# Optimization experiments

Hardware: AMD Instinct MI355X
Metric: run time of the kernel (lower is better)

## Reference

```python
import jax, jax.numpy as jnp
import numpy as np

HIDDEN = 1024
HEADS = 16
HEAD_DIM = HIDDEN // HEADS  # 64
BLOCK = 1024  # block_size; seq_len > BLOCK triggers ring path
B, S = 1, 4096


def setup_inputs() -> dict:
    key = jax.random.key(0)
    k0, k1, k2, k3, k4 = jax.random.split(key, 5)
    w_scale = 0.02
    return {
        "hidden_states": jax.random.normal(k0, (B, S, HIDDEN), dtype=jnp.float32),
        # weights stored [in, out]; applied as x @ W (equivalent to nn.Linear with W.T)
        "w_q": jax.random.normal(k1, (HIDDEN, HIDDEN), dtype=jnp.float32) * w_scale,
        "w_k": jax.random.normal(k2, (HIDDEN, HIDDEN), dtype=jnp.float32) * w_scale,
        "w_v": jax.random.normal(k3, (HIDDEN, HIDDEN), dtype=jnp.float32) * w_scale,
        "w_o": jax.random.normal(k4, (HIDDEN, HIDDEN), dtype=jnp.float32) * w_scale,
    }


def _ring_attention(q, k, v, block, scale):
    # q,k,v: [B, H, S, D]. Faithful to the torch module: each KV block subtracts
    # its OWN local max (no running-max rescale); exp-sums and weighted-V are
    # accumulated additively across KV blocks, then normalized once at the end.
    b, h, s, d = q.shape
    nb = s // block
    kb = jnp.moveaxis(k.reshape(b, h, nb, block, d), 2, 0)  # [nb, B, H, block, D]
    vb = jnp.moveaxis(v.reshape(b, h, nb, block, d), 2, 0)

    def step(carry, kv):
        num, den = carry
        k_blk, v_blk = kv
        s_blk = jnp.einsum("bhqd,bhkd->bhqk", q, k_blk) * scale  # [B,H,S,block]
        m = jnp.max(s_blk, axis=-1, keepdims=True)               # local max only
        e = jnp.exp(s_blk - m)
        num = num + jnp.einsum("bhqk,bhkd->bhqd", e, v_blk)
        den = den + jnp.sum(e, axis=-1, keepdims=True)
        return (num, den), None

    init = (jnp.zeros_like(q), jnp.zeros((b, h, s, 1), dtype=q.dtype))
    (num, den), _ = jax.lax.scan(step, init, (kb, vb))
    return num / den


def reference(hidden_states, w_q, w_k, w_v, w_o):
    b, s, _ = hidden_states.shape
    q = (hidden_states @ w_q).reshape(b, s, HEADS, HEAD_DIM).transpose(0, 2, 1, 3)
    k = (hidden_states @ w_k).reshape(b, s, HEADS, HEAD_DIM).transpose(0, 2, 1, 3)
    v = (hidden_states @ w_v).reshape(b, s, HEADS, HEAD_DIM).transpose(0, 2, 1, 3)
    scale = HEAD_DIM ** -0.5
    out = _ring_attention(q, k, v, BLOCK, scale)          # [B,H,S,D]
    out = out.transpose(0, 2, 1, 3).reshape(b, s, HIDDEN)  # [B,S,hidden]
    return out @ w_o
```

## Files before the change

### kernel.cpp

```cpp
#include <hip/hip_runtime.h>
#include <hip/hip_bf16.h>

typedef __bf16 bf16;
typedef bf16 bf16x2 __attribute__((ext_vector_type(2)));
typedef bf16 bf16x4 __attribute__((ext_vector_type(4)));
typedef bf16 bf16x8 __attribute__((ext_vector_type(8)));
typedef float f32x4 __attribute__((ext_vector_type(4)));

#define HID 1024
#define NHEADS 16
#define HD 64
#define SEQ 4096

__device__ __forceinline__ void gll16(const void* g, void* l) {
  __builtin_amdgcn_global_load_lds(
      (const __attribute__((address_space(1))) void*)g,
      (__attribute__((address_space(3))) void*)l, 16, 0, 0);
}

__device__ __forceinline__ float fast_exp2(float x) {
#if __has_builtin(__builtin_amdgcn_exp2f)
  return __builtin_amdgcn_exp2f(x);
#else
  return __expf(x * 0.6931471805599453f);
#endif
}

__global__ __launch_bounds__(256)
void prep_kernel(const float* __restrict__ X,
                 const float* __restrict__ Wq, const float* __restrict__ Wk,
                 const float* __restrict__ Wv, const float* __restrict__ Wo,
                 bf16* __restrict__ Xb, bf16* __restrict__ Wt)
{
  const int z = blockIdx.z, t = threadIdx.x, bx = blockIdx.x;
  if (z == 0) {
    const float4* src = (const float4*)X;
    const int gid = bx * 256 + t;
    #pragma unroll
    for (int i = 0; i < 16; ++i) {
      float4 v = src[gid + i * 65536];
      bf16x4 o = {(bf16)v.x, (bf16)v.y, (bf16)v.z, (bf16)v.w};
      *(bf16x4*)&Xb[(size_t)(gid + i * 65536) * 4] = o;
    }
  } else {
    const float* W = (z == 1) ? Wq : (z == 2) ? Wk : (z == 3) ? Wv : Wo;
    bf16* dst = Wt + (size_t)(z - 1) * HID * HID;
    const float scale = (z == 1) ? 0.18033688011112042f : 1.0f;
    __shared__ bf16 T[64][68];
    const int tr = (bx >> 4) * 64, tc = (bx & 15) * 64;
    #pragma unroll
    for (int p = 0; p < 4; ++p) {
      int row = (t >> 4) + p * 16;
      float4 v = *(const float4*)&W[(size_t)(tr + row) * HID + tc + (t & 15) * 4];
      T[row][(t & 15) * 4 + 0] = (bf16)(v.x * scale);
      T[row][(t & 15) * 4 + 1] = (bf16)(v.y * scale);
      T[row][(t & 15) * 4 + 2] = (bf16)(v.z * scale);
      T[row][(t & 15) * 4 + 3] = (bf16)(v.w * scale);
    }
    __syncthreads();
    #pragma unroll
    for (int p = 0; p < 4; ++p) {
      int rp = (t >> 4) + p * 16;
      int cb = (t & 15) * 4;
      bf16x4 o = {T[cb + 0][rp], T[cb + 1][rp], T[cb + 2][rp], T[cb + 3][rp]};
      *(bf16x4*)&dst[(size_t)(tc + rp) * HID + tr + cb] = o;
    }
  }
}

__global__ __launch_bounds__(256)
void qkv_gemm(const bf16* __restrict__ A, const bf16* __restrict__ Wt,
              bf16* __restrict__ Qg, bf16* __restrict__ Kg,
              bf16* __restrict__ Vt)
{
  __shared__ bf16 sbuf[16384];
  bf16* As = sbuf;
  bf16* Bs = sbuf + 8192;

  const int t = threadIdx.x, lane = t & 63, w = t >> 6;
  const int z = blockIdx.z;
  const int n0 = blockIdx.x * 128, m0 = blockIdx.y * 128;
  const bf16* Bt = Wt + (size_t)z * HID * HID;
  const int wm = (w & 1) * 64, wn = (w >> 1) * 64;
  const int fr = lane & 15, quad = lane >> 4;

  f32x4 acc[4][4] = {};

  const int sr = lane >> 3;
  const int sc = ((lane & 7) - sr) & 7;
  const bf16* ga = A  + (size_t)(m0 + w * 32 + sr) * HID + sc * 8;
  const bf16* gb = Bt + (size_t)(n0 + w * 32 + sr) * HID + sc * 8;

  for (int k0 = 0; k0 < HID; k0 += 64) {
    __syncthreads();
    #pragma unroll
    for (int c = 0; c < 4; ++c) {
      gll16(ga + (size_t)(c * 8) * HID + k0, As + (w * 32 + c * 8) * 64);
      gll16(gb + (size_t)(c * 8) * HID + k0, Bs + (w * 32 + c * 8) * 64);
    }
    __syncthreads();
    #pragma unroll
    for (int ks = 0; ks < 2; ++ks) {
      bf16x8 af[4], bg[4];
      #pragma unroll
      for (int i = 0; i < 4; ++i)
        af[i] = *(const bf16x8*)&As[(wm + i * 16 + fr) * 64 +
                                    ((ks * 4 + quad + fr) & 7) * 8];
      #pragma unroll
      for (int i = 0; i < 4; ++i)
        bg[i] = *(const bf16x8*)&Bs[(wn + i * 16 + fr) * 64 +
                                    ((ks * 4 + quad + fr) & 7) * 8];
      #pragma unroll
      for (int mi = 0; mi < 4; ++mi)
        #pragma unroll
        for (int ni = 0; ni < 4; ++ni)
          acc[mi][ni] = __builtin_amdgcn_mfma_f32_16x16x32_bf16(
              af[mi], bg[ni], acc[mi][ni], 0, 0, 0);
    }
  }

  if (z < 2) {
    bf16* C = z ? Kg : Qg;
    #pragma unroll
    for (int mi = 0; mi < 4; ++mi)
      #pragma unroll
      for (int ni = 0; ni < 4; ++ni)
        #pragma unroll
        for (int r = 0; r < 4; ++r)
          C[(size_t)(m0 + wm + mi * 16 + quad * 4 + r) * HID +
            n0 + wn + ni * 16 + fr] = (bf16)acc[mi][ni][r];
  } else {
    __syncthreads();
    #pragma unroll
    for (int mi = 0; mi < 4; ++mi)
      #pragma unroll
      for (int ni = 0; ni < 4; ++ni)
        #pragma unroll
        for (int r = 0; r < 4; ++r) {
          int row = wn + ni * 16 + fr;
          int col = wm + mi * 16 + quad * 4 + r;
          int colS = (col + 8 * (row & 15)) & 127;
          sbuf[row * 128 + colS] = (bf16)acc[mi][ni][r];
        }
    __syncthreads();
    const int row = t >> 1, cb = (t & 1) * 64;
    #pragma unroll
    for (int j = 0; j < 8; ++j) {
      int c0 = (cb + j * 8 + 8 * (row & 15)) & 127;
      *(bf16x8*)&Vt[(size_t)(n0 + row) * SEQ + m0 + cb + j * 8] =
          *(const bf16x8*)&sbuf[row * 128 + c0];
    }
  }
}

__global__ __launch_bounds__(256)
void oproj_gemm(const bf16* __restrict__ A, const bf16* __restrict__ Bt,
                float* __restrict__ C)
{
  __shared__ bf16 sbuf[16384];
  bf16* As = sbuf;
  bf16* Bs = sbuf + 8192;

  const int t = threadIdx.x, lane = t & 63, w = t >> 6;
  const int n0 = blockIdx.x * 128, m0 = blockIdx.y * 128;
  const int wm = (w & 1) * 64, wn = (w >> 1) * 64;
  const int fr = lane & 15, quad = lane >> 4;

  f32x4 acc[4][4] = {};

  const int sr = lane >> 3;
  const int sc = ((lane & 7) - sr) & 7;
  const bf16* ga = A  + (size_t)(m0 + w * 32 + sr) * HID + sc * 8;
  const bf16* gb = Bt + (size_t)(n0 + w * 32 + sr) * HID + sc * 8;

  for (int k0 = 0; k0 < HID; k0 += 64) {
    __syncthreads();
    #pragma unroll
    for (int c = 0; c < 4; ++c) {
      gll16(ga + (size_t)(c * 8) * HID + k0, As + (w * 32 + c * 8) * 64);
      gll16(gb + (size_t)(c * 8) * HID + k0, Bs + (w * 32 + c * 8) * 64);
    }
    __syncthreads();
    #pragma unroll
    for (int ks = 0; ks < 2; ++ks) {
      bf16x8 af[4], bg[4];
      #pragma unroll
      for (int i = 0; i < 4; ++i)
        af[i] = *(const bf16x8*)&As[(wm + i * 16 + fr) * 64 +
                                    ((ks * 4 + quad + fr) & 7) * 8];
      #pragma unroll
      for (int i = 0; i < 4; ++i)
        bg[i] = *(const bf16x8*)&Bs[(wn + i * 16 + fr) * 64 +
                                    ((ks * 4 + quad + fr) & 7) * 8];
      #pragma unroll
      for (int mi = 0; mi < 4; ++mi)
        #pragma unroll
        for (int ni = 0; ni < 4; ++ni)
          acc[mi][ni] = __builtin_amdgcn_mfma_f32_16x16x32_bf16(
              af[mi], bg[ni], acc[mi][ni], 0, 0, 0);
    }
  }

  #pragma unroll
  for (int mi = 0; mi < 4; ++mi)
    #pragma unroll
    for (int ni = 0; ni < 4; ++ni)
      #pragma unroll
      for (int r = 0; r < 4; ++r)
        C[(size_t)(m0 + wm + mi * 16 + quad * 4 + r) * HID +
          n0 + wn + ni * 16 + fr] = acc[mi][ni][r];
}

#define THR_L2 12.0f

__global__ __launch_bounds__(256, 4)
void attn6(const bf16* __restrict__ Q, const bf16* __restrict__ K,
           const bf16* __restrict__ Vt, float* __restrict__ Num,
           float* __restrict__ Den)
{
  __shared__ bf16 Ks[2][4096];
  __shared__ bf16 Vs[2][4096];
  __shared__ bf16 Ps[4][1024];

  const int t = threadIdx.x, lane = t & 63, w = t >> 6;
  const int h = blockIdx.y, q0 = blockIdx.x * 128, half = blockIdx.z;
  const int fr = lane & 15, quad = lane >> 4;

  bf16x8 bq[2][2];
  #pragma unroll
  for (int qf = 0; qf < 2; ++qf)
    #pragma unroll
    for (int ks = 0; ks < 2; ++ks)
      bq[qf][ks] = *(const bf16x8*)&Q[(size_t)(q0 + w * 32 + qf * 16 + fr) * HID
                                      + h * 64 + ks * 32 + quad * 8];

  const int sr = lane >> 3;
  const int sc = ((lane & 7) - sr) & 7;
  const bf16* gk = K  + (size_t)(half * 2048 + w * 16 + sr) * HID + h * 64 + sc * 8;
  const bf16* gv = Vt + (size_t)(h * 64 + w * 16 + sr) * SEQ + half * 2048 + sc * 8;

  #pragma unroll
  for (int j = 0; j < 2; ++j) {
    gll16(gk + (size_t)(j * 8) * HID, &Ks[0][(w * 16 + j * 8) * 64]);
    gll16(gv + (size_t)(j * 8) * SEQ, &Vs[0][(w * 16 + j * 8) * 64]);
  }

  f32x4 accN[2][4] = {};
  f32x4 accO[2][4] = {};
  float m_used[2] = {-3e38f, -3e38f}, m_true[2] = {-3e38f, -3e38f};
  float l_i[2] = {0.f, 0.f}, den[2] = {0.f, 0.f};

  __syncthreads();

  for (int kk = 0; kk < 32; ++kk) {
    const int buf = kk & 1;
    if (kk < 31) {
      const size_t key0n = (size_t)(kk + 1) * 64;
      #pragma unroll
      for (int j = 0; j < 2; ++j) {
        gll16(gk + (key0n + j * 8) * HID, &Ks[buf ^ 1][(w * 16 + j * 8) * 64]);
        gll16(gv + key0n + (size_t)(j * 8) * SEQ,
              &Vs[buf ^ 1][(w * 16 + j * 8) * 64]);
      }
    }

    bf16x8 ak[4][2];
    #pragma unroll
    for (int mt = 0; mt < 4; ++mt)
      #pragma unroll
      for (int ks = 0; ks < 2; ++ks)
        ak[mt][ks] = *(const bf16x8*)&Ks[buf][(mt * 16 + fr) * 64 +
                                             ((ks * 4 + quad + fr) & 7) * 8];

    f32x4 s[2][4];
    #pragma unroll
    for (int qf = 0; qf < 2; ++qf)
      #pragma unroll
      for (int mt = 0; mt < 4; ++mt) {
        f32x4 z = {};
        z = __builtin_amdgcn_mfma_f32_16x16x32_bf16(ak[mt][0], bq[qf][0], z, 0, 0, 0);
        z = __builtin_amdgcn_mfma_f32_16x16x32_bf16(ak[mt][1], bq[qf][1], z, 0, 0, 0);
        s[qf][mt] = z;
      }

    bf16x8 bp[2][2];
    #pragma unroll
    for (int qf = 0; qf < 2; ++qf) {
      float mx0 = fmaxf(fmaxf(s[qf][0][0], s[qf][0][1]), fmaxf(s[qf][0][2], s[qf][0][3]));
      float mx1 = fmaxf(fmaxf(s[qf][1][0], s[qf][1][1]), fmaxf(s[qf][1][2], s[qf][1][3]));
      float mx2 = fmaxf(fmaxf(s[qf][2][0], s[qf][2][1]), fmaxf(s[qf][2][2], s[qf][2][3]));
      float mx3 = fmaxf(fmaxf(s[qf][3][0], s[qf][3][1]), fmaxf(s[qf][3][2], s[qf][3][3]));
      float mx = fmaxf(fmaxf(mx0, mx1), fmaxf(mx2, mx3));
      mx = fmaxf(mx, __shfl_xor(mx, 16));
      mx = fmaxf(mx, __shfl_xor(mx, 32));
      m_true[qf] = fmaxf(m_true[qf], mx);

      if (__any(mx > m_used[qf] + THR_L2)) {
        const float mn = fmaxf(m_used[qf], mx);
        const float a = fast_exp2(m_used[qf] - mn);
        m_used[qf] = mn;
        l_i[qf] *= a;
        #pragma unroll
        for (int dt = 0; dt < 4; ++dt) accO[qf][dt] *= a;
      }

      float sum = 0.f;
      const int prow = fr * 64;
      #pragma unroll
      for (int mt = 0; mt < 4; ++mt) {
        float p0 = fast_exp2(s[qf][mt][0] - m_used[qf]);
        float p1 = fast_exp2(s[qf][mt][1] - m_used[qf]);
        float p2 = fast_exp2(s[qf][mt][2] - m_used[qf]);
        float p3 = fast_exp2(s[qf][mt][3] - m_used[qf]);
        sum += (p0 + p1) + (p2 + p3);
        bf16x4 pv = {(bf16)p0, (bf16)p1, (bf16)p2, (bf16)p3};
        *(bf16x4*)&Ps[w][prow + ((mt * 2 + (quad >> 1) + fr) & 7) * 8 +
                         (quad & 1) * 4] = pv;
      }
      sum += __shfl_xor(sum, 16);
      sum += __shfl_xor(sum, 32);
      l_i[qf] += sum;

      #pragma unroll
      for (int ks = 0; ks < 2; ++ks)
        bp[qf][ks] = *(const bf16x8*)&Ps[w][fr * 64 +
                                            ((ks * 4 + quad + fr) & 7) * 8];
    }

    #pragma unroll
    for (int ks = 0; ks < 2; ++ks)
      #pragma unroll
      for (int dt = 0; dt < 4; ++dt) {
        bf16x8 av = *(const bf16x8*)&Vs[buf][(dt * 16 + fr) * 64 +
                                            ((ks * 4 + quad + fr) & 7) * 8];
        accO[0][dt] = __builtin_amdgcn_mfma_f32_16x16x32_bf16(av, bp[0][ks], accO[0][dt], 0, 0, 0);
        accO[1][dt] = __builtin_amdgcn_mfma_f32_16x16x32_bf16(av, bp[1][ks], accO[1][dt], 0, 0, 0);
      }

    if ((kk & 15) == 15) {
      #pragma unroll
      for (int qf = 0; qf < 2; ++qf) {
        const float c = fast_exp2(m_used[qf] - m_true[qf]);
        den[qf] += l_i[qf] * c;
        #pragma unroll
        for (int dt = 0; dt < 4; ++dt)
          #pragma unroll
          for (int r = 0; r < 4; ++r) accN[qf][dt][r] += accO[qf][dt][r] * c;
        #pragma unroll
        for (int dt = 0; dt < 4; ++dt) accO[qf][dt] = (f32x4){0.f, 0.f, 0.f, 0.f};
        l_i[qf] = 0.f; m_used[qf] = -3e38f; m_true[qf] = -3e38f;
      }
    }
    __syncthreads();
  }

  float* numH = Num + (size_t)half * SEQ * HID;
  #pragma unroll
  for (int qf = 0; qf < 2; ++qf) {
    const int qrow = q0 + w * 32 + qf * 16 + fr;
    const size_t orow = (size_t)qrow * HID + h * 64;
    #pragma unroll
    for (int dt = 0; dt < 4; ++dt)
      *(f32x4*)&numH[orow + dt * 16 + quad * 4] = accN[qf][dt];
    if (quad == 0)
      Den[((size_t)half * 16 + h) * SEQ + qrow] = den[qf];
  }
}

__global__ __launch_bounds__(256)
void combine_kernel(const float* __restrict__ Num, const float* __restrict__ Den,
                    bf16* __restrict__ Og)
{
  const int gid = blockIdx.x * 256 + threadIdx.x;
  const int idx = gid * 4;
  const int row = idx >> 10, col = idx & 1023, h = col >> 6;
  const float d0 = Den[(size_t)h * SEQ + row];
  const float d1 = Den[((size_t)16 + h) * SEQ + row];
  const float inv = 1.0f / (d0 + d1);
  f32x4 a = *(const f32x4*)&Num[idx];
  f32x4 b = *(const f32x4*)&Num[(size_t)SEQ * HID + idx];
  bf16x4 o = {(bf16)((a[0] + b[0]) * inv), (bf16)((a[1] + b[1]) * inv),
              (bf16)((a[2] + b[2]) * inv), (bf16)((a[3] + b[3]) * inv)};
  *(bf16x4*)&Og[idx] = o;
}

__global__ __launch_bounds__(256, 2)
void attn5(const bf16* __restrict__ Q, const bf16* __restrict__ K,
           const bf16* __restrict__ Vt, bf16* __restrict__ O)
{
  __shared__ bf16 Ks[2][4096];
  __shared__ bf16 Vs[2][4096];
  __shared__ bf16 Ps[4][1024];

  const int t = threadIdx.x, lane = t & 63, w = t >> 6;
  const int h = blockIdx.y, q0 = blockIdx.x * 128;
  const int fr = lane & 15, quad = lane >> 4;

  bf16x8 bq[2][2];
  #pragma unroll
  for (int qf = 0; qf < 2; ++qf)
    #pragma unroll
    for (int ks = 0; ks < 2; ++ks)
      bq[qf][ks] = *(const bf16x8*)&Q[(size_t)(q0 + w * 32 + qf * 16 + fr) * HID
                                      + h * 64 + ks * 32 + quad * 8];

  const int sr = lane >> 3;
  const int sc = ((lane & 7) - sr) & 7;
  const bf16* gk = K  + (size_t)(w * 16 + sr) * HID + h * 64 + sc * 8;
  const bf16* gv = Vt + (size_t)(h * 64 + w * 16 + sr) * SEQ + sc * 8;

  #pragma unroll
  for (int j = 0; j < 2; ++j) {
    gll16(gk + (size_t)(j * 8) * HID, &Ks[0][(w * 16 + j * 8) * 64]);
    gll16(gv + (size_t)(j * 8) * SEQ, &Vs[0][(w * 16 + j * 8) * 64]);
  }

  f32x4 accN[2][4] = {};
  f32x4 accO[2][4] = {};
  float m_used[2] = {-3e38f, -3e38f}, m_true[2] = {-3e38f, -3e38f};
  float l_i[2] = {0.f, 0.f}, den[2] = {0.f, 0.f};

  __syncthreads();

  for (int kk = 0; kk < 64; ++kk) {
    const int buf = kk & 1;
    if (kk < 63) {
      const size_t key0n = (size_t)(kk + 1) * 64;
      #pragma unroll
      for (int j = 0; j < 2; ++j) {
        gll16(gk + (key0n + j * 8) * HID, &Ks[buf ^ 1][(w * 16 + j * 8) * 64]);
        gll16(gv + key0n + (size_t)(j * 8) * SEQ,
              &Vs[buf ^ 1][(w * 16 + j * 8) * 64]);
      }
    }

    bf16x8 ak[4][2];
    #pragma unroll
    for (int mt = 0; mt < 4; ++mt)
      #pragma unroll
      for (int ks = 0; ks < 2; ++ks)
        ak[mt][ks] = *(const bf16x8*)&Ks[buf][(mt * 16 + fr) * 64 +
                                             ((ks * 4 + quad + fr) & 7) * 8];

    f32x4 s[2][4];
    #pragma unroll
    for (int qf = 0; qf < 2; ++qf)
      #pragma unroll
      for (int mt = 0; mt < 4; ++mt) {
        f32x4 z = {};
        z = __builtin_amdgcn_mfma_f32_16x16x32_bf16(ak[mt][0], bq[qf][0], z, 0, 0, 0);
        z = __builtin_amdgcn_mfma_f32_16x16x32_bf16(ak[mt][1], bq[qf][1], z, 0, 0, 0);
        s[qf][mt] = z;
      }

    bf16x8 bp[2][2];
    #pragma unroll
    for (int qf = 0; qf < 2; ++qf) {
      float mx0 = fmaxf(fmaxf(s[qf][0][0], s[qf][0][1]), fmaxf(s[qf][0][2], s[qf][0][3]));
      float mx1 = fmaxf(fmaxf(s[qf][1][0], s[qf][1][1]), fmaxf(s[qf][1][2], s[qf][1][3]));
      float mx2 = fmaxf(fmaxf(s[qf][2][0], s[qf][2][1]), fmaxf(s[qf][2][2], s[qf][2][3]));
      float mx3 = fmaxf(fmaxf(s[qf][3][0], s[qf][3][1]), fmaxf(s[qf][3][2], s[qf][3][3]));
      float mx = fmaxf(fmaxf(mx0, mx1), fmaxf(mx2, mx3));
      mx = fmaxf(mx, __shfl_xor(mx, 16));
      mx = fmaxf(mx, __shfl_xor(mx, 32));
      m_true[qf] = fmaxf(m_true[qf], mx);

      if (__any(mx > m_used[qf] + THR_L2)) {
        const float mn = fmaxf(m_used[qf], mx);
        const float a = fast_exp2(m_used[qf] - mn);
        m_used[qf] = mn;
        l_i[qf] *= a;
        #pragma unroll
        for (int dt = 0; dt < 4; ++dt) accO[qf][dt] *= a;
      }

      float sum = 0.f;
      const int prow = fr * 64;
      #pragma unroll
      for (int mt = 0; mt < 4; ++mt) {
        float p0 = fast_exp2(s[qf][mt][0] - m_used[qf]);
        float p1 = fast_exp2(s[qf][mt][1] - m_used[qf]);
        float p2 = fast_exp2(s[qf][mt][2] - m_used[qf]);
        float p3 = fast_exp2(s[qf][mt][3] - m_used[qf]);
        sum += (p0 + p1) + (p2 + p3);
        bf16x4 pv = {(bf16)p0, (bf16)p1, (bf16)p2, (bf16)p3};
        *(bf16x4*)&Ps[w][prow + ((mt * 2 + (quad >> 1) + fr) & 7) * 8 +
                         (quad & 1) * 4] = pv;
      }
      sum += __shfl_xor(sum, 16);
      sum += __shfl_xor(sum, 32);
      l_i[qf] += sum;

      #pragma unroll
      for (int ks = 0; ks < 2; ++ks)
        bp[qf][ks] = *(const bf16x8*)&Ps[w][fr * 64 +
                                            ((ks * 4 + quad + fr) & 7) * 8];
    }

    #pragma unroll
    for (int ks = 0; ks < 2; ++ks)
      #pragma unroll
      for (int dt = 0; dt < 4; ++dt) {
        bf16x8 av = *(const bf16x8*)&Vs[buf][(dt * 16 + fr) * 64 +
                                            ((ks * 4 + quad + fr) & 7) * 8];
        accO[0][dt] = __builtin_amdgcn_mfma_f32_16x16x32_bf16(av, bp[0][ks], accO[0][dt], 0, 0, 0);
        accO[1][dt] = __builtin_amdgcn_mfma_f32_16x16x32_bf16(av, bp[1][ks], accO[1][dt], 0, 0, 0);
      }

    if ((kk & 15) == 15) {
      #pragma unroll
      for (int qf = 0; qf < 2; ++qf) {
        const float c = fast_exp2(m_used[qf] - m_true[qf]);
        den[qf] += l_i[qf] * c;
        #pragma unroll
        for (int dt = 0; dt < 4; ++dt)
          #pragma unroll
          for (int r = 0; r < 4; ++r) accN[qf][dt][r] += accO[qf][dt][r] * c;
        #pragma unroll
        for (int dt = 0; dt < 4; ++dt) accO[qf][dt] = (f32x4){0.f, 0.f, 0.f, 0.f};
        l_i[qf] = 0.f; m_used[qf] = -3e38f; m_true[qf] = -3e38f;
      }
    }
    __syncthreads();
  }

  #pragma unroll
  for (int qf = 0; qf < 2; ++qf) {
    const float inv = 1.0f / den[qf];
    const size_t orow = (size_t)(q0 + w * 32 + qf * 16 + fr) * HID + h * 64;
    #pragma unroll
    for (int dt = 0; dt < 4; ++dt) {
      bf16x4 ov = {(bf16)(accN[qf][dt][0] * inv), (bf16)(accN[qf][dt][1] * inv),
                   (bf16)(accN[qf][dt][2] * inv), (bf16)(accN[qf][dt][3] * inv)};
      *(bf16x4*)&O[orow + dt * 16 + quad * 4] = ov;
    }
  }
}

extern "C" void kernel_launch(void* const* d_in, const int* in_sizes, int n_in,
                              void* d_out, int out_size, void* d_ws, size_t ws_size,
                              hipStream_t stream)
{
  const float* X  = (const float*)d_in[0];
  const float* Wq = (const float*)d_in[1];
  const float* Wk = (const float*)d_in[2];
  const float* Wv = (const float*)d_in[3];
  const float* Wo = (const float*)d_in[4];
  float* out = (float*)d_out;

  const size_t MB = 1024 * 1024;
  bf16*  Xb  = (bf16*)d_ws;
  bf16*  Wt  = (bf16*)((char*)d_ws + 8  * MB);
  bf16*  Qg  = (bf16*)((char*)d_ws + 16 * MB);
  bf16*  Kg  = (bf16*)((char*)d_ws + 24 * MB);
  bf16*  Vtg = (bf16*)((char*)d_ws + 32 * MB);
  bf16*  Og  = (bf16*)((char*)d_ws + 40 * MB);
  float* Num = (float*)((char*)d_ws + 48 * MB);
  float* Den = (float*)((char*)d_ws + 80 * MB);

  prep_kernel<<<dim3(256, 1, 5), 256, 0, stream>>>(X, Wq, Wk, Wv, Wo, Xb, Wt);
  qkv_gemm<<<dim3(HID / 128, SEQ / 128, 3), 256, 0, stream>>>(Xb, Wt, Qg, Kg, Vtg);
  if (ws_size >= 81 * MB) {
    attn6<<<dim3(SEQ / 128, NHEADS, 2), 256, 0, stream>>>(Qg, Kg, Vtg, Num, Den);
    combine_kernel<<<dim3(SEQ * HID / 1024, 1, 1), 256, 0, stream>>>(Num, Den, Og);
  } else {
    attn5<<<dim3(SEQ / 128, NHEADS), 256, 0, stream>>>(Qg, Kg, Vtg, Og);
  }
  oproj_gemm<<<dim3(HID / 128, SEQ / 128), 256, 0, stream>>>(
      Og, Wt + (size_t)3 * HID * HID, out);
}
```

Before: 268.3 us.

## Split attention into four KV-block partitions with direct global loads and bf16 partials

The attention kernel now splits the keys into four 1024-key blocks, one grid z-slice each, instead of two halves, so each workgroup runs 16 iterations and the grid holds twice as many workgroups. K and V tiles are read straight from global memory into registers, which drops the LDS double-buffering and the per-iteration barriers and lets occupancy rise to 6. Each partition writes a normalized bf16 partial output plus its block denominator, and a new combine kernel weights the four partials. The cost is uncoalesced, unshared global loads of K/V across waves and some extra bf16 rounding in the partials.

New measurement: 899.3 us. 3.35x slower.

```diff
diff --git a/kernel.cpp b/kernel.cpp
--- a/kernel.cpp
+++ b/kernel.cpp
@@ -213,17 +213,15 @@
 
 #define THR_L2 12.0f
 
-__global__ __launch_bounds__(256, 4)
-void attn6(const bf16* __restrict__ Q, const bf16* __restrict__ K,
-           const bf16* __restrict__ Vt, float* __restrict__ Num,
+__global__ __launch_bounds__(256, 6)
+void attn7(const bf16* __restrict__ Q, const bf16* __restrict__ K,
+           const bf16* __restrict__ Vt, bf16* __restrict__ Opart,
            float* __restrict__ Den)
 {
-  __shared__ bf16 Ks[2][4096];
-  __shared__ bf16 Vs[2][4096];
   __shared__ bf16 Ps[4][1024];
 
   const int t = threadIdx.x, lane = t & 63, w = t >> 6;
-  const int h = blockIdx.y, q0 = blockIdx.x * 128, half = blockIdx.z;
+  const int h = blockIdx.y, q0 = blockIdx.x * 128, qtr = blockIdx.z;
   const int fr = lane & 15, quad = lane >> 4;
 
   bf16x8 bq[2][2];
@@ -234,43 +232,23 @@
       bq[qf][ks] = *(const bf16x8*)&Q[(size_t)(q0 + w * 32 + qf * 16 + fr) * HID
                                       + h * 64 + ks * 32 + quad * 8];
 
-  const int sr = lane >> 3;
-  const int sc = ((lane & 7) - sr) & 7;
-  const bf16* gk = K  + (size_t)(half * 2048 + w * 16 + sr) * HID + h * 64 + sc * 8;
-  const bf16* gv = Vt + (size_t)(h * 64 + w * 16 + sr) * SEQ + half * 2048 + sc * 8;
-
-  #pragma unroll
-  for (int j = 0; j < 2; ++j) {
-    gll16(gk + (size_t)(j * 8) * HID, &Ks[0][(w * 16 + j * 8) * 64]);
-    gll16(gv + (size_t)(j * 8) * SEQ, &Vs[0][(w * 16 + j * 8) * 64]);
-  }
-
-  f32x4 accN[2][4] = {};
+  const bf16* kb = K  + (size_t)(qtr * 1024 + fr) * HID + h * 64 + quad * 8;
+  const bf16* vb = Vt + (size_t)(h * 64 + fr) * SEQ + qtr * 1024 + quad * 8;
+
   f32x4 accO[2][4] = {};
   float m_used[2] = {-3e38f, -3e38f}, m_true[2] = {-3e38f, -3e38f};
-  float l_i[2] = {0.f, 0.f}, den[2] = {0.f, 0.f};
-
-  __syncthreads();
-
-  for (int kk = 0; kk < 32; ++kk) {
-    const int buf = kk & 1;
-    if (kk < 31) {
-      const size_t key0n = (size_t)(kk + 1) * 64;
-      #pragma unroll
-      for (int j = 0; j < 2; ++j) {
-        gll16(gk + (key0n + j * 8) * HID, &Ks[buf ^ 1][(w * 16 + j * 8) * 64]);
-        gll16(gv + key0n + (size_t)(j * 8) * SEQ,
-              &Vs[buf ^ 1][(w * 16 + j * 8) * 64]);
-      }
-    }
+  float l_i[2] = {0.f, 0.f};
+
+  for (int kk = 0; kk < 16; ++kk) {
+    const int key0 = kk * 64;
 
     bf16x8 ak[4][2];
     #pragma unroll
     for (int mt = 0; mt < 4; ++mt)
       #pragma unroll
       for (int ks = 0; ks < 2; ++ks)
-        ak[mt][ks] = *(const bf16x8*)&Ks[buf][(mt * 16 + fr) * 64 +
-                                             ((ks * 4 + quad + fr) & 7) * 8];
+        ak[mt][ks] = *(const bf16x8*)&kb[(size_t)(key0 + mt * 16) * HID +
+                                         ks * 32];
 
     f32x4 s[2][4];
     #pragma unroll
@@ -282,6 +260,14 @@
         z = __builtin_amdgcn_mfma_f32_16x16x32_bf16(ak[mt][1], bq[qf][1], z, 0, 0, 0);
         s[qf][mt] = z;
       }
+
+    bf16x8 av[4][2];
+    #pragma unroll
+    for (int dt = 0; dt < 4; ++dt)
+      #pragma unroll
+      for (int ks = 0; ks < 2; ++ks)
+        av[dt][ks] = *(const bf16x8*)&vb[(size_t)(dt * 16) * SEQ +
+                                         key0 + ks * 32];
 
     bf16x8 bp[2][2];
     #pragma unroll
@@ -331,57 +317,51 @@
     for (int ks = 0; ks < 2; ++ks)
       #pragma unroll
       for (int dt = 0; dt < 4; ++dt) {
-        bf16x8 av = *(const bf16x8*)&Vs[buf][(dt * 16 + fr) * 64 +
-                                            ((ks * 4 + quad + fr) & 7) * 8];
-        accO[0][dt] = __builtin_amdgcn_mfma_f32_16x16x32_bf16(av, bp[0][ks], accO[0][dt], 0, 0, 0);
-        accO[1][dt] = __builtin_amdgcn_mfma_f32_16x16x32_bf16(av, bp[1][ks], accO[1][dt], 0, 0, 0);
-      }
-
-    if ((kk & 15) == 15) {
-      #pragma unroll
-      for (int qf = 0; qf < 2; ++qf) {
-        const float c = fast_exp2(m_used[qf] - m_true[qf]);
-        den[qf] += l_i[qf] * c;
-        #pragma unroll
-        for (int dt = 0; dt < 4; ++dt)
-          #pragma unroll
-          for (int r = 0; r < 4; ++r) accN[qf][dt][r] += accO[qf][dt][r] * c;
-        #pragma unroll
-        for (int dt = 0; dt < 4; ++dt) accO[qf][dt] = (f32x4){0.f, 0.f, 0.f, 0.f};
-        l_i[qf] = 0.f; m_used[qf] = -3e38f; m_true[qf] = -3e38f;
-      }
-    }
-    __syncthreads();
-  }
-
-  float* numH = Num + (size_t)half * SEQ * HID;
+        accO[0][dt] = __builtin_amdgcn_mfma_f32_16x16x32_bf16(av[dt][ks], bp[0][ks], accO[0][dt], 0, 0, 0);
+        accO[1][dt] = __builtin_amdgcn_mfma_f32_16x16x32_bf16(av[dt][ks], bp[1][ks], accO[1][dt], 0, 0, 0);
+      }
+  }
+
+  bf16* Oq = Opart + (size_t)qtr * SEQ * HID;
   #pragma unroll
   for (int qf = 0; qf < 2; ++qf) {
     const int qrow = q0 + w * 32 + qf * 16 + fr;
+    const float inv = 1.0f / l_i[qf];
     const size_t orow = (size_t)qrow * HID + h * 64;
     #pragma unroll
-    for (int dt = 0; dt < 4; ++dt)
-      *(f32x4*)&numH[orow + dt * 16 + quad * 4] = accN[qf][dt];
+    for (int dt = 0; dt < 4; ++dt) {
+      bf16x4 ov = {(bf16)(accO[qf][dt][0] * inv), (bf16)(accO[qf][dt][1] * inv),
+                   (bf16)(accO[qf][dt][2] * inv), (bf16)(accO[qf][dt][3] * inv)};
+      *(bf16x4*)&Oq[orow + dt * 16 + quad * 4] = ov;
+    }
     if (quad == 0)
-      Den[((size_t)half * 16 + h) * SEQ + qrow] = den[qf];
+      Den[((size_t)qtr * 16 + h) * SEQ + qrow] =
+          l_i[qf] * fast_exp2(m_used[qf] - m_true[qf]);
   }
 }
 
 __global__ __launch_bounds__(256)
-void combine_kernel(const float* __restrict__ Num, const float* __restrict__ Den,
-                    bf16* __restrict__ Og)
-{
-  const int gid = blockIdx.x * 256 + threadIdx.x;
-  const int idx = gid * 4;
-  const int row = idx >> 10, col = idx & 1023, h = col >> 6;
-  const float d0 = Den[(size_t)h * SEQ + row];
-  const float d1 = Den[((size_t)16 + h) * SEQ + row];
-  const float inv = 1.0f / (d0 + d1);
-  f32x4 a = *(const f32x4*)&Num[idx];
-  f32x4 b = *(const f32x4*)&Num[(size_t)SEQ * HID + idx];
-  bf16x4 o = {(bf16)((a[0] + b[0]) * inv), (bf16)((a[1] + b[1]) * inv),
-              (bf16)((a[2] + b[2]) * inv), (bf16)((a[3] + b[3]) * inv)};
-  *(bf16x4*)&Og[idx] = o;
+void combine4_kernel(const bf16* __restrict__ Opart,
+                     const float* __restrict__ Den, bf16* __restrict__ Og)
+{
+  const size_t gid = (size_t)blockIdx.x * 256 + threadIdx.x;
+  const size_t idx = gid * 8;
+  const int row = (int)(idx >> 10), h = ((int)idx & 1023) >> 6;
+  float d[4];
+  #pragma unroll
+  for (int q = 0; q < 4; ++q) d[q] = Den[((size_t)q * 16 + h) * SEQ + row];
+  const float inv = 1.0f / (d[0] + d[1] + d[2] + d[3]);
+  float acc[8] = {};
+  #pragma unroll
+  for (int q = 0; q < 4; ++q) {
+    bf16x8 o = *(const bf16x8*)&Opart[(size_t)q * SEQ * HID + idx];
+    const float wq = d[q] * inv;
+    #pragma unroll
+    for (int j = 0; j < 8; ++j) acc[j] += (float)o[j] * wq;
+  }
+  bf16x8 r = {(bf16)acc[0], (bf16)acc[1], (bf16)acc[2], (bf16)acc[3],
+              (bf16)acc[4], (bf16)acc[5], (bf16)acc[6], (bf16)acc[7]};
+  *(bf16x8*)&Og[idx] = r;
 }
 
 __global__ __launch_bounds__(256, 2)
@@ -555,14 +535,14 @@
   bf16*  Kg  = (bf16*)((char*)d_ws + 24 * MB);
   bf16*  Vtg = (bf16*)((char*)d_ws + 32 * MB);
   bf16*  Og  = (bf16*)((char*)d_ws + 40 * MB);
-  float* Num = (float*)((char*)d_ws + 48 * MB);
-  float* Den = (float*)((char*)d_ws + 80 * MB);
+  bf16*  Opart = (bf16*)((char*)d_ws + 48 * MB);
+  float* Den   = (float*)((char*)d_ws + 80 * MB);
 
   prep_kernel<<<dim3(256, 1, 5), 256, 0, stream>>>(X, Wq, Wk, Wv, Wo, Xb, Wt);
   qkv_gemm<<<dim3(HID / 128, SEQ / 128, 3), 256, 0, stream>>>(Xb, Wt, Qg, Kg, Vtg);
   if (ws_size >= 81 * MB) {
-    attn6<<<dim3(SEQ / 128, NHEADS, 2), 256, 0, stream>>>(Qg, Kg, Vtg, Num, Den);
-    combine_kernel<<<dim3(SEQ * HID / 1024, 1, 1), 256, 0, stream>>>(Num, Den, Og);
+    attn7<<<dim3(SEQ / 128, NHEADS, 4), 256, 0, stream>>>(Qg, Kg, Vtg, Opart, Den);
+    combine4_kernel<<<dim3(SEQ * HID / 2048, 1, 1), 256, 0, stream>>>(Opart, Den, Og);
   } else {
     attn5<<<dim3(SEQ / 128, NHEADS), 256, 0, stream>>>(Qg, Kg, Vtg, Og);
   }
```
